# Kernel optimization log

Measured on AMD Instinct MI355X. Metric: run time of the kernel, lower is better.

## Reference

```python
import jax, jax.numpy as jnp
import numpy as np

N = 50000      # nodes
E = 800000     # edges (before self-loops)
IN = 256       # in_channels
HID = 128      # hidden_channels
OUT = 128      # out_channels
NEG_SLOPE = 0.2
EPS = 1e-16


def setup_inputs() -> dict:
    key = jax.random.key(0)
    ks = jax.random.split(key, 16)
    p = lambda k, shape: jax.random.normal(k, shape, jnp.float32) * 0.1
    return {
        "x": jax.random.normal(ks[0], (N, IN), jnp.float32),
        "edge_index": jax.random.randint(ks[1], (2, E), 0, N, dtype=jnp.int64),
        # semantic MLP
        "W1": p(ks[2], (IN, HID)), "b1": jnp.zeros((HID,), jnp.float32),
        "W2": p(ks[3], (HID, HID)), "b2": jnp.zeros((HID,), jnp.float32),
        # gat1: HID -> HID//2, heads=4, concat -> 2*HID
        "g1_W": p(ks[4], (HID, 4 * (HID // 2))),
        "g1_as": p(ks[5], (4, HID // 2)), "g1_ad": p(ks[6], (4, HID // 2)),
        "g1_b": jnp.zeros((4 * (HID // 2),), jnp.float32),
        # gat2: 2*HID -> OUT, heads=2, mean -> OUT
        "g2_W": p(ks[7], (2 * HID, 2 * OUT)),
        "g2_as": p(ks[8], (2, OUT)), "g2_ad": p(ks[9], (2, OUT)),
        "g2_b": jnp.zeros((OUT,), jnp.float32),
        # gat3: OUT -> OUT, heads=1, mean -> OUT
        "g3_W": p(ks[10], (OUT, OUT)),
        "g3_as": p(ks[11], (1, OUT)), "g3_ad": p(ks[12], (1, OUT)),
        "g3_b": jnp.zeros((OUT,), jnp.float32),
    }


def _gat(h_in, src, dst, W, a_src, a_dst, bias, heads, concat, n):
    # Linear projection into heads: [n, H, C]
    h = (h_in @ W).reshape(n, heads, -1)
    alpha_s = jnp.sum(h * a_src[None], axis=-1)  # [n, H]
    alpha_d = jnp.sum(h * a_dst[None], axis=-1)  # [n, H]
    e = jax.nn.leaky_relu(alpha_s[src] + alpha_d[dst], NEG_SLOPE)  # [E', H]
    # segment softmax over edges grouped by destination node
    m = jax.ops.segment_max(e, dst, num_segments=n)
    ex = jnp.exp(e - m[dst])
    denom = jax.ops.segment_sum(ex, dst, num_segments=n)
    alpha = ex / (denom[dst] + EPS)  # [E', H]
    msg = h[src] * alpha[..., None]  # [E', H, C]
    out = jax.ops.segment_sum(msg, dst, num_segments=n)  # [n, H, C]
    out = out.reshape(n, -1) if concat else out.mean(axis=1)
    return out + bias


def reference(x, edge_index, W1, b1, W2, b2,
              g1_W, g1_as, g1_ad, g1_b,
              g2_W, g2_as, g2_ad, g2_b,
              g3_W, g3_as, g3_ad, g3_b):
    n = x.shape[0]
    # PyG GATConv add_self_loops=True: append self-loop edges once
    loops = jnp.arange(n, dtype=edge_index.dtype)
    src = jnp.concatenate([edge_index[0], loops])
    dst = jnp.concatenate([edge_index[1], loops])
    # semantic MLP (inference: dropout = identity)
    h = jax.nn.relu(x @ W1 + b1)
    h = jax.nn.relu(h @ W2 + b2)
    h = jax.nn.elu(_gat(h, src, dst, g1_W, g1_as, g1_ad, g1_b, 4, True, n))
    h = jax.nn.elu(_gat(h, src, dst, g2_W, g2_as, g2_ad, g2_b, 2, False, n))
    h = _gat(h, src, dst, g3_W, g3_as, g3_ad, g3_b, 1, False, n)
    return h
```

## Files before the change

### kernel.cpp

```cpp
#include <hip/hip_runtime.h>
#include <math.h>


#define NEG_SLOPE 0.2f
#define EPS_DEN 1e-16f

typedef __attribute__((ext_vector_type(8))) short short8;
typedef __attribute__((ext_vector_type(4))) float f32x4;
typedef __attribute__((ext_vector_type(2))) float f32x2;
typedef __attribute__((ext_vector_type(4))) unsigned short u16x4;

__device__ inline unsigned short f2b(float f) {
  unsigned u = __builtin_bit_cast(unsigned, f);
  unsigned r = (u + 0x7fffu + ((u >> 16) & 1u)) >> 16;
  return (unsigned short)r;
}
__device__ inline float b2f(unsigned short u) {
  return __builtin_bit_cast(float, (unsigned)u << 16);
}

__device__ inline void glds16(const void* g, void* l) {
  __builtin_amdgcn_global_load_lds(
      (const __attribute__((address_space(1))) void*)g,
      (__attribute__((address_space(3))) void*)l, 16, 0, 0);
}

__device__ inline f32x2 pk_fma(f32x2 a, f32x2 b, f32x2 c) {
  f32x2 d;
  asm("v_pk_fma_f32 %0, %1, %2, %3" : "=v"(d) : "v"(a), "v"(b), "v"(c));
  return d;
}

__device__ inline void accum8(f32x2 acc2[4], const short8 r, float w) {
  const f32x2 wv = {w, w};
  const unsigned* u = (const unsigned*)&r;
#pragma unroll
  for (int p = 0; p < 4; p++) {
    const unsigned lo = u[p] << 16;
    const unsigned hi = u[p] & 0xffff0000u;
    f32x2 val = {__builtin_bit_cast(float, lo), __builtin_bit_cast(float, hi)};
    acc2[p] = pk_fma(val, wv, acc2[p]);
  }
}

template <int H>
__device__ inline void loadH(const float* p, float* v) {
  if constexpr (H == 4) {
    float4 t = *(const float4*)p;
    v[0] = t.x; v[1] = t.y; v[2] = t.z; v[3] = t.w;
  } else if constexpr (H == 2) {
    float2 t = *(const float2*)p;
    v[0] = t.x; v[1] = t.y;
  } else {
    v[0] = *p;
  }
}

template <int ACT, int OBF, int H, int CC>
__global__ __launch_bounds__(256) void mfma_gemm(
    const unsigned short* __restrict__ A, const unsigned short* __restrict__ Bt,
    const float* __restrict__ bias, float* __restrict__ Cf,
    unsigned short* __restrict__ Cb, const float* __restrict__ a_s,
    const float* __restrict__ a_d, float* __restrict__ alS,
    float* __restrict__ alD, int n, int K, int M) {
  __shared__ unsigned short As[128 * 64];
  __shared__ unsigned short Bs[128 * 64];

  const int tid = threadIdx.x;
  const int w = tid >> 6, lane = tid & 63;
  const int row0 = blockIdx.x * 128, col0 = blockIdx.y * 128;
  const int lr = lane >> 3, lg = lane & 7;
  const int lm = lane & 15, kg = lane >> 4;
  const int wm = (w >> 1) * 64, wn = (w & 1) * 64;

  f32x4 acc[4][4];
#pragma unroll
  for (int i = 0; i < 4; i++)
#pragma unroll
    for (int j = 0; j < 4; j++) acc[i][j] = {0.f, 0.f, 0.f, 0.f};

  const int swz = (lg ^ lr) << 3;

  for (int k0 = 0; k0 < K; k0 += 64) {
    __syncthreads();
#pragma unroll
    for (int it = 0; it < 4; it++) {
      const int r = w * 32 + it * 8;
      glds16(A + (size_t)(row0 + r + lr) * K + k0 + swz, &As[r * 64]);
      glds16(Bt + (size_t)(col0 + r + lr) * K + k0 + swz, &Bs[r * 64]);
    }
    __syncthreads();

#pragma unroll
    for (int kh = 0; kh < 2; kh++) {
      const int sw = ((kh * 4 + kg) ^ (lm & 7)) << 3;
      short8 aF[4], bF[4];
#pragma unroll
      for (int i = 0; i < 4; i++) {
        aF[i] = *(const short8*)&As[(wm + i * 16 + lm) * 64 + sw];
        bF[i] = *(const short8*)&Bs[(wn + i * 16 + lm) * 64 + sw];
      }
#pragma unroll
      for (int i = 0; i < 4; i++)
#pragma unroll
        for (int j = 0; j < 4; j++)
          acc[i][j] = __builtin_amdgcn_mfma_f32_16x16x32_bf16(
              aF[i], bF[j], acc[i][j], 0, 0, 0);
    }
  }

  const int r4 = kg * 4;

  if constexpr (H > 0) {
    const int head = (col0 + wn) / CC;
    const int ch0 = (col0 + wn) % CC;
    float asv[4], adv[4];
#pragma unroll
    for (int j = 0; j < 4; j++) {
      asv[j] = a_s[head * CC + ch0 + j * 16 + lm];
      adv[j] = a_d[head * CC + ch0 + j * 16 + lm];
    }
    float psA[4][4], pdA[4][4];
#pragma unroll
    for (int i = 0; i < 4; i++) {
#pragma unroll
      for (int r = 0; r < 4; r++) {
        float ps = 0.f, pd = 0.f;
#pragma unroll
        for (int j = 0; j < 4; j++) {
          ps += acc[i][j][r] * asv[j];
          pd += acc[i][j][r] * adv[j];
        }
#pragma unroll
        for (int off = 1; off < 16; off <<= 1) {
          ps += __shfl_xor(ps, off, 64);
          pd += __shfl_xor(pd, off, 64);
        }
        psA[i][r] = ps;
        pdA[i][r] = pd;
      }
    }
    if constexpr (CC == 64) {
      if (lm == 0) {
#pragma unroll
        for (int i = 0; i < 4; i++)
#pragma unroll
          for (int r = 0; r < 4; r++) {
            const int row = row0 + wm + i * 16 + r4 + r;
            if (row < n) {
              alS[(size_t)row * H + head] = psA[i][r];
              alD[(size_t)row * H + head] = pdA[i][r];
            }
          }
      }
    } else {
      __shared__ float redS[4][64];
      __shared__ float redD[4][64];
      if (lm == 0) {
#pragma unroll
        for (int i = 0; i < 4; i++)
#pragma unroll
          for (int r = 0; r < 4; r++) {
            redS[w][i * 16 + r4 + r] = psA[i][r];
            redD[w][i * 16 + r4 + r] = pdA[i][r];
          }
      }
      __syncthreads();
      if ((w & 1) == 0) {
        const int row = row0 + wm + lane;
        if (row < n) {
          const int hd = col0 / CC;
          alS[(size_t)row * H + hd] = redS[w][lane] + redS[w + 1][lane];
          alD[(size_t)row * H + hd] = redD[w][lane] + redD[w + 1][lane];
        }
      }
    }
  }

#pragma unroll
  for (int j = 0; j < 4; j++) {
    const int col = col0 + wn + j * 16 + lm;
    const float bv = bias ? bias[col] : 0.f;
#pragma unroll
    for (int i = 0; i < 4; i++) {
#pragma unroll
      for (int r = 0; r < 4; r++) {
        const int row = row0 + wm + i * 16 + r4 + r;
        if (row < n) {
          float v = acc[i][j][r] + bv;
          if (ACT == 1) v = v > 0.f ? v : 0.f;
          if (OBF)
            Cb[(size_t)row * M + col] = f2b(v);
          else
            Cf[(size_t)row * M + col] = v;
        }
      }
    }
  }
}

__global__ __launch_bounds__(256) void mlp_g1_kernel(
    const unsigned short* __restrict__ X, const unsigned short* __restrict__ W1t,
    const float* __restrict__ b1, const unsigned short* __restrict__ W2t,
    const float* __restrict__ b2, const unsigned short* __restrict__ G1Wt,
    const float* __restrict__ a_s, const float* __restrict__ a_d,
    float* __restrict__ alS, float* __restrict__ alD,
    unsigned short* __restrict__ Pb, int n) {
  __shared__ unsigned short As[128 * 64];
  __shared__ unsigned short Bs[128 * 64];
  __shared__ unsigned short H1s[128 * 136];

  const int tid = threadIdx.x;
  const int w = tid >> 6, lane = tid & 63;
  const int row0 = blockIdx.x * 128;
  const int lr = lane >> 3, lg = lane & 7;
  const int lm = lane & 15, kg = lane >> 4;
  const int wm = (w >> 1) * 64, wn = (w & 1) * 64;
  const int swz = (lg ^ lr) << 3;
  const int r4 = kg * 4;

  f32x4 acc[4][4];
#pragma unroll
  for (int i = 0; i < 4; i++)
#pragma unroll
    for (int j = 0; j < 4; j++) acc[i][j] = {0.f, 0.f, 0.f, 0.f};

  for (int k0 = 0; k0 < 256; k0 += 64) {
    __syncthreads();
#pragma unroll
    for (int it = 0; it < 4; it++) {
      const int r = w * 32 + it * 8;
      glds16(X + (size_t)(row0 + r + lr) * 256 + k0 + swz, &As[r * 64]);
      glds16(W1t + (size_t)(r + lr) * 256 + k0 + swz, &Bs[r * 64]);
    }
    __syncthreads();
#pragma unroll
    for (int kh = 0; kh < 2; kh++) {
      const int sw = ((kh * 4 + kg) ^ (lm & 7)) << 3;
      short8 aF[4], bF[4];
#pragma unroll
      for (int i = 0; i < 4; i++) {
        aF[i] = *(const short8*)&As[(wm + i * 16 + lm) * 64 + sw];
        bF[i] = *(const short8*)&Bs[(wn + i * 16 + lm) * 64 + sw];
      }
#pragma unroll
      for (int i = 0; i < 4; i++)
#pragma unroll
        for (int j = 0; j < 4; j++)
          acc[i][j] = __builtin_amdgcn_mfma_f32_16x16x32_bf16(
              aF[i], bF[j], acc[i][j], 0, 0, 0);
    }
  }

#pragma unroll
  for (int j = 0; j < 4; j++) {
    const int col = wn + j * 16 + lm;
    const float bv = b1[col];
#pragma unroll
    for (int i = 0; i < 4; i++) {
#pragma unroll
      for (int r = 0; r < 4; r++) {
        const int lrow = wm + i * 16 + r4 + r;
        float v = acc[i][j][r] + bv;
        v = v > 0.f ? v : 0.f;
        H1s[lrow * 136 + col] = f2b(v);
      }
    }
  }
#pragma unroll
  for (int i = 0; i < 4; i++)
#pragma unroll
    for (int j = 0; j < 4; j++) acc[i][j] = {0.f, 0.f, 0.f, 0.f};
  __syncthreads();

  for (int k0 = 0; k0 < 128; k0 += 64) {
    __syncthreads();
#pragma unroll
    for (int it = 0; it < 4; it++) {
      const int r = w * 32 + it * 8;
      glds16(W2t + (size_t)(r + lr) * 128 + k0 + swz, &Bs[r * 64]);
    }
    __syncthreads();
#pragma unroll
    for (int kh = 0; kh < 2; kh++) {
      const int swB = ((kh * 4 + kg) ^ (lm & 7)) << 3;
      const int kofs = k0 + (kh * 4 + kg) * 8;
      short8 aF[4], bF[4];
#pragma unroll
      for (int i = 0; i < 4; i++) {
        aF[i] = *(const short8*)&H1s[(wm + i * 16 + lm) * 136 + kofs];
        bF[i] = *(const short8*)&Bs[(wn + i * 16 + lm) * 64 + swB];
      }
#pragma unroll
      for (int i = 0; i < 4; i++)
#pragma unroll
        for (int j = 0; j < 4; j++)
          acc[i][j] = __builtin_amdgcn_mfma_f32_16x16x32_bf16(
              aF[i], bF[j], acc[i][j], 0, 0, 0);
    }
  }

  __syncthreads();
#pragma unroll
  for (int j = 0; j < 4; j++) {
    const int col = wn + j * 16 + lm;
    const float bv = b2[col];
#pragma unroll
    for (int i = 0; i < 4; i++) {
#pragma unroll
      for (int r = 0; r < 4; r++) {
        const int lrow = wm + i * 16 + r4 + r;
        float v = acc[i][j][r] + bv;
        v = v > 0.f ? v : 0.f;
        H1s[lrow * 136 + col] = f2b(v);
      }
    }
  }
  __syncthreads();

  for (int c = 0; c < 2; c++) {
#pragma unroll
    for (int i = 0; i < 4; i++)
#pragma unroll
      for (int j = 0; j < 4; j++) acc[i][j] = {0.f, 0.f, 0.f, 0.f};

    for (int k0 = 0; k0 < 128; k0 += 64) {
      __syncthreads();
#pragma unroll
      for (int it = 0; it < 4; it++) {
        const int r = w * 32 + it * 8;
        glds16(G1Wt + (size_t)(c * 128 + r + lr) * 128 + k0 + swz,
               &Bs[r * 64]);
      }
      __syncthreads();
#pragma unroll
      for (int kh = 0; kh < 2; kh++) {
        const int swB = ((kh * 4 + kg) ^ (lm & 7)) << 3;
        const int kofs = k0 + (kh * 4 + kg) * 8;
        short8 aF[4], bF[4];
#pragma unroll
        for (int i = 0; i < 4; i++) {
          aF[i] = *(const short8*)&H1s[(wm + i * 16 + lm) * 136 + kofs];
          bF[i] = *(const short8*)&Bs[(wn + i * 16 + lm) * 64 + swB];
        }
#pragma unroll
        for (int i = 0; i < 4; i++)
#pragma unroll
          for (int j = 0; j < 4; j++)
            acc[i][j] = __builtin_amdgcn_mfma_f32_16x16x32_bf16(
                aF[i], bF[j], acc[i][j], 0, 0, 0);
      }
    }

    {
      const int head = c * 2 + (wn >> 6);
      float asv[4], adv[4];
#pragma unroll
      for (int j = 0; j < 4; j++) {
        asv[j] = a_s[head * 64 + j * 16 + lm];
        adv[j] = a_d[head * 64 + j * 16 + lm];
      }
#pragma unroll
      for (int i = 0; i < 4; i++) {
#pragma unroll
        for (int r = 0; r < 4; r++) {
          float ps = 0.f, pd = 0.f;
#pragma unroll
          for (int j = 0; j < 4; j++) {
            ps += acc[i][j][r] * asv[j];
            pd += acc[i][j][r] * adv[j];
          }
#pragma unroll
          for (int off = 1; off < 16; off <<= 1) {
            ps += __shfl_xor(ps, off, 64);
            pd += __shfl_xor(pd, off, 64);
          }
          if (lm == 0) {
            const int row = row0 + wm + i * 16 + r4 + r;
            if (row < n) {
              alS[(size_t)row * 4 + head] = ps;
              alD[(size_t)row * 4 + head] = pd;
            }
          }
        }
      }
    }

#pragma unroll
    for (int j = 0; j < 4; j++) {
      const int col = c * 128 + wn + j * 16 + lm;
#pragma unroll
      for (int i = 0; i < 4; i++) {
#pragma unroll
        for (int r = 0; r < 4; r++) {
          const int row = row0 + wm + i * 16 + r4 + r;
          if (row < n) Pb[(size_t)row * 256 + col] = f2b(acc[i][j][r]);
        }
      }
    }
  }
}

struct PrepArgs {
  const float* x; unsigned short* xb; long long nx;
  const float* W[5]; unsigned short* Wt[5];
  int K[5], M[5], t0[6];
  int* deg; int* rank; const int* edst; int E; int N;
};

__global__ __launch_bounds__(256) void fused_prep_kernel(PrepArgs a) {
  const int tid = threadIdx.x, bid = blockIdx.x, nb = gridDim.x;
  const long long gt = (long long)bid * 256 + tid;
  const long long gsz = (long long)nb * 256;
  __shared__ float tt[32][33];

  const long long etot = (long long)a.E + a.N;
  for (long long i = gt; i < etot; i += gsz) {
    int d = (i < a.E) ? __builtin_nontemporal_load(a.edst + i)
                      : (int)(i - a.E);
    if ((unsigned)d < (unsigned)a.N)
      a.rank[i] = atomicAdd(&a.deg[d], 1);
  }
  for (long long i = gt * 4; i < a.nx; i += gsz * 4) {
    float4 v = *(const float4*)(a.x + i);
    u16x4 u = {f2b(v.x), f2b(v.y), f2b(v.z), f2b(v.w)};
    *(u16x4*)(a.xb + i) = u;
  }
  for (int t = bid; t < a.t0[5]; t += nb) {
    int di = 0;
    while (t >= a.t0[di + 1]) di++;
    const int local = t - a.t0[di];
    const int K = a.K[di], M = a.M[di], mtiles = M / 32;
    const int mb = (local % mtiles) * 32, kb = (local / mtiles) * 32;
    const float* W = a.W[di];
    unsigned short* Wt = a.Wt[di];
    const int tx = tid & 31, ty = tid >> 5;
    __syncthreads();
#pragma unroll
    for (int i = 0; i < 4; i++)
      tt[ty + i * 8][tx] = W[(size_t)(kb + ty + i * 8) * M + mb + tx];
    __syncthreads();
#pragma unroll
    for (int i = 0; i < 4; i++)
      Wt[(size_t)(mb + ty + i * 8) * K + kb + tx] = f2b(tt[tx][ty + i * 8]);
  }
}

__global__ __launch_bounds__(256) void block_reduce_kernel(
    const int* __restrict__ deg, int* __restrict__ bsum, int n) {
  __shared__ int s[256];
  const int t = threadIdx.x, i = blockIdx.x * 256 + t;
  s[t] = (i < n) ? deg[i] : 0;
  __syncthreads();
#pragma unroll
  for (int off = 128; off; off >>= 1) {
    if (t < off) s[t] += s[t + off];
    __syncthreads();
  }
  if (t == 0) bsum[blockIdx.x] = s[0];
}

__global__ __launch_bounds__(256) void scan_bsums_kernel(int* __restrict__ bsum,
                                                         int nb) {
  __shared__ int s[256];
  const int t = threadIdx.x;
  const int v = (t < nb) ? bsum[t] : 0;
  s[t] = v;
  __syncthreads();
#pragma unroll
  for (int off = 1; off < 256; off <<= 1) {
    int a = (t >= off) ? s[t - off] : 0;
    __syncthreads();
    s[t] += a;
    __syncthreads();
  }
  if (t < nb) bsum[t] = s[t] - v;
}

__global__ __launch_bounds__(256) void scan_final_kernel(
    const int* __restrict__ deg, const int* __restrict__ bsumx,
    int* __restrict__ rowptr, int n) {
  __shared__ int s[256];
  const int t = threadIdx.x, i = blockIdx.x * 256 + t;
  const int v = (i < n) ? deg[i] : 0;
  s[t] = v;
  __syncthreads();
#pragma unroll
  for (int off = 1; off < 256; off <<= 1) {
    int a = (t >= off) ? s[t - off] : 0;
    __syncthreads();
    s[t] += a;
    __syncthreads();
  }
  if (i < n) {
    const int base = bsumx[blockIdx.x];
    rowptr[i] = base + s[t] - v;
    if (i == n - 1) rowptr[n] = base + s[t];
  }
}

__global__ void scatter_kernel(const int* __restrict__ esrc,
                               const int* __restrict__ edst,
                               const int* __restrict__ rank,
                               const int* __restrict__ rowptr,
                               int* __restrict__ csr_src, int E, int n) {
  int i = blockIdx.x * blockDim.x + threadIdx.x;
  int tot = E + n;
  if (i >= tot) return;
  int s, d;
  if (i < E) {
    s = __builtin_nontemporal_load(esrc + i);
    d = __builtin_nontemporal_load(edst + i);
  } else {
    s = d = i - E;
  }
  if ((unsigned)d >= (unsigned)n || (unsigned)s >= (unsigned)n) return;
  int pos = rowptr[d] + __builtin_nontemporal_load(rank + i);
  csr_src[pos] = s;
}

template <int H, int C, bool CONCAT, int ACT, int OBF>
__global__ __launch_bounds__(256) void gat_fused_kernel(
    const unsigned short* __restrict__ proj, const float* __restrict__ alpha_s,
    const float* __restrict__ alpha_d, const int* __restrict__ rowptr,
    const int* __restrict__ csr_src, const float* __restrict__ bias,
    void* __restrict__ out, int n) {
  constexpr int HC = H * C;
  constexpr int ROWSPAN = HC / 8;
  constexpr int EDGES = 64 / ROWSPAN;
  constexpr int WLANES = C / 8;

  __shared__ float exs[4][64 * H];
  __shared__ int sids[4][64];

  const int wv = threadIdx.x >> 6;
  const int wid = (blockIdx.x * blockDim.x + threadIdx.x) >> 6;
  const int lane = threadIdx.x & 63;
  if (wid >= n) return;
  const int dst = wid;
  const int eslot = lane / ROWSPAN;
  const int sl = lane % ROWSPAN;
  const int h_lane = (sl * 8) / C;
  float* myex = &exs[wv][0];
  int* mysid = &sids[wv][0];

  float adv[H];
  loadH<H>(alpha_d + (size_t)dst * H, adv);
  const int rs = rowptr[dst], re = rowptr[dst + 1];

  float denomp[H];
#pragma unroll
  for (int h = 0; h < H; h++) denomp[h] = 0.f;
  f32x2 acc2[4];
#pragma unroll
  for (int p = 0; p < 4; p++) acc2[p] = {0.f, 0.f};

  const unsigned short* prow = proj + sl * 8;

  for (int base = rs; base < re; base += 64) {
    const int cnt = min(64, re - base);
    if (lane < cnt) {
      const int s = __builtin_nontemporal_load(csr_src + base + lane);
      mysid[lane] = s;
      float as[H];
      loadH<H>(alpha_s + (size_t)s * H, as);
#pragma unroll
      for (int h = 0; h < H; h++) {
        float e = as[h] + adv[h];
        e = e > 0.f ? e : NEG_SLOPE * e;
        const float ex = __expf(e);
        denomp[h] += ex;
        myex[lane * H + h] = ex;
      }
    }
    __builtin_amdgcn_wave_barrier();
    int j = eslot;
    for (; j + EDGES < cnt; j += 2 * EDGES) {
      const int s0 = mysid[j];
      const int s1 = mysid[j + EDGES];
      const float w0 = myex[j * H + h_lane];
      const float w1 = myex[(j + EDGES) * H + h_lane];
      const short8 r0 = *(const short8*)(prow + (size_t)s0 * HC);
      const short8 r1 = *(const short8*)(prow + (size_t)s1 * HC);
      accum8(acc2, r0, w0);
      accum8(acc2, r1, w1);
    }
    for (; j < cnt; j += EDGES) {
      const int s0 = mysid[j];
      const float w0 = myex[j * H + h_lane];
      const short8 r0 = *(const short8*)(prow + (size_t)s0 * HC);
      accum8(acc2, r0, w0);
    }
    __builtin_amdgcn_wave_barrier();
  }

  float acc[8];
#pragma unroll
  for (int p = 0; p < 4; p++) {
    acc[2 * p] = acc2[p].x;
    acc[2 * p + 1] = acc2[p].y;
  }

#pragma unroll
  for (int off = 32; off; off >>= 1)
#pragma unroll
    for (int h = 0; h < H; h++)
      denomp[h] += __shfl_xor(denomp[h], off, 64);
#pragma unroll
  for (int off = ROWSPAN; off < 64; off <<= 1)
#pragma unroll
    for (int k = 0; k < 8; k++) acc[k] += __shfl_xor(acc[k], off, 64);

  const float inv = 1.f / (denomp[h_lane] + EPS_DEN);
  float v[8];
#pragma unroll
  for (int k = 0; k < 8; k++) v[k] = acc[k] * inv;

  if (!CONCAT && H == 2) {
#pragma unroll
    for (int k = 0; k < 8; k++) v[k] += __shfl_xor(v[k], 16, 64);
  }

  if (CONCAT) {
    if (eslot != 0) return;
    const int c0 = sl * 8;
    float vv[8];
#pragma unroll
    for (int k = 0; k < 8; k++) {
      float t = v[k] + bias[c0 + k];
      if (ACT == 1) t = t > 0.f ? t : (__expf(t) - 1.f);
      vv[k] = t;
    }
    if (OBF) {
      short8 o;
#pragma unroll
      for (int k = 0; k < 8; k++) o[k] = (short)f2b(vv[k]);
      __builtin_nontemporal_store(
          o, (short8*)((unsigned short*)out + (size_t)dst * HC + c0));
    } else {
      float* op = (float*)out + (size_t)dst * HC + c0;
      f32x4 o0 = {vv[0], vv[1], vv[2], vv[3]};
      f32x4 o1 = {vv[4], vv[5], vv[6], vv[7]};
      __builtin_nontemporal_store(o0, (f32x4*)op);
      __builtin_nontemporal_store(o1, (f32x4*)(op + 4));
    }
  } else {
    if (eslot != 0 || sl >= WLANES) return;
    const int c0 = sl * 8;
    const float invH = 1.f / (float)H;
    float vv[8];
#pragma unroll
    for (int k = 0; k < 8; k++) {
      float t = v[k] * invH + bias[c0 + k];
      if (ACT == 1) t = t > 0.f ? t : (__expf(t) - 1.f);
      vv[k] = t;
    }
    if (OBF) {
      short8 o;
#pragma unroll
      for (int k = 0; k < 8; k++) o[k] = (short)f2b(vv[k]);
      __builtin_nontemporal_store(
          o, (short8*)((unsigned short*)out + (size_t)dst * C + c0));
    } else {
      float* op = (float*)out + (size_t)dst * C + c0;
      f32x4 o0 = {vv[0], vv[1], vv[2], vv[3]};
      f32x4 o1 = {vv[4], vv[5], vv[6], vv[7]};
      __builtin_nontemporal_store(o0, (f32x4*)op);
      __builtin_nontemporal_store(o1, (f32x4*)(op + 4));
    }
  }
}

extern "C" void kernel_launch(void* const* d_in, const int* in_sizes, int n_in,
                              void* d_out, int out_size, void* d_ws,
                              size_t ws_size, hipStream_t stream) {
  const float* x    = (const float*)d_in[0];
  const int*   ei   = (const int*)d_in[1];
  const float* W1   = (const float*)d_in[2];
  const float* b1   = (const float*)d_in[3];
  const float* W2   = (const float*)d_in[4];
  const float* b2   = (const float*)d_in[5];
  const float* g1W  = (const float*)d_in[6];
  const float* g1as = (const float*)d_in[7];
  const float* g1ad = (const float*)d_in[8];
  const float* g1b  = (const float*)d_in[9];
  const float* g2W  = (const float*)d_in[10];
  const float* g2as = (const float*)d_in[11];
  const float* g2ad = (const float*)d_in[12];
  const float* g2b  = (const float*)d_in[13];
  const float* g3W  = (const float*)d_in[14];
  const float* g3as = (const float*)d_in[15];
  const float* g3ad = (const float*)d_in[16];
  const float* g3b  = (const float*)d_in[17];

  const int N = in_sizes[0] / 256;
  const int E = in_sizes[1] / 2;
  const int Etot = E + N;
  const int NT = (N + 127) / 128;
  const int NP = NT * 128;
  const int NB = (N + 255) / 256;

  char* p = (char*)d_ws;
  unsigned short* Pb  = (unsigned short*)p; p += (size_t)NP * 256 * 2;
  unsigned short* xb  = (unsigned short*)p; p += (size_t)NP * 256 * 2;
  unsigned short* h2b = (unsigned short*)p; p += (size_t)NP * 128 * 2;
  unsigned short* W1t = (unsigned short*)p; p += (size_t)128 * 256 * 2;
  unsigned short* W2t = (unsigned short*)p; p += (size_t)128 * 128 * 2;
  unsigned short* g1Wt = (unsigned short*)p; p += (size_t)256 * 128 * 2;
  unsigned short* g2Wt = (unsigned short*)p; p += (size_t)256 * 256 * 2;
  unsigned short* g3Wt = (unsigned short*)p; p += (size_t)128 * 128 * 2;
  float* alB = (float*)p; p += (size_t)N * 14 * 4;
  float* alS1 = alB;
  float* alD1 = alB + (size_t)4 * N;
  float* alS2 = alB + (size_t)8 * N;
  float* alD2 = alB + (size_t)10 * N;
  float* alS3 = alB + (size_t)12 * N;
  float* alD3 = alB + (size_t)13 * N;
  int* deg    = (int*)p; p += (size_t)N * 4;
  int* rowptr = (int*)p; p += (size_t)(N + 1) * 4;
  int* bsum   = (int*)p; p += 256 * 4;
  int* rank   = (int*)p; p += (size_t)Etot * 4;
  int* csrsrc = (int*)p;

  const int* esrc = ei;
  const int* edst = ei + E;
  unsigned short* act1b = xb;
  unsigned short* act2b = h2b;

  hipMemsetAsync(deg, 0, (size_t)N * 4, stream);

  PrepArgs pa;
  pa.x = x; pa.xb = xb; pa.nx = (long long)N * 256;
  pa.W[0] = W1;  pa.Wt[0] = W1t;  pa.K[0] = 256; pa.M[0] = 128;
  pa.W[1] = W2;  pa.Wt[1] = W2t;  pa.K[1] = 128; pa.M[1] = 128;
  pa.W[2] = g1W; pa.Wt[2] = g1Wt; pa.K[2] = 128; pa.M[2] = 256;
  pa.W[3] = g2W; pa.Wt[3] = g2Wt; pa.K[3] = 256; pa.M[3] = 256;
  pa.W[4] = g3W; pa.Wt[4] = g3Wt; pa.K[4] = 128; pa.M[4] = 128;
  pa.t0[0] = 0;
  for (int i = 0; i < 5; i++)
    pa.t0[i + 1] = pa.t0[i] + (pa.K[i] / 32) * (pa.M[i] / 32);
  pa.deg = deg; pa.rank = rank; pa.edst = edst; pa.E = E; pa.N = N;
  fused_prep_kernel<<<512, 256, 0, stream>>>(pa);

  block_reduce_kernel<<<NB, 256, 0, stream>>>(deg, bsum, N);
  scan_bsums_kernel<<<1, 256, 0, stream>>>(bsum, NB);
  scan_final_kernel<<<NB, 256, 0, stream>>>(deg, bsum, rowptr, N);
  scatter_kernel<<<(Etot + 255) / 256, 256, 0, stream>>>(esrc, edst, rank,
                                                         rowptr, csrsrc, E, N);

  mlp_g1_kernel<<<NT, 256, 0, stream>>>(xb, W1t, b1, W2t, b2, g1Wt, g1as,
                                        g1ad, alS1, alD1, Pb, N);

  gat_fused_kernel<4, 64, true, 1, 1><<<(N + 3) / 4, 256, 0, stream>>>(
      Pb, alS1, alD1, rowptr, csrsrc, g1b, act1b, N);

  mfma_gemm<0, 1, 2, 128><<<dim3(NT, 2), 256, 0, stream>>>(
      act1b, g2Wt, nullptr, nullptr, Pb, g2as, g2ad, alS2, alD2, N, 256, 256);
  gat_fused_kernel<2, 128, false, 1, 1><<<(N + 3) / 4, 256, 0, stream>>>(
      Pb, alS2, alD2, rowptr, csrsrc, g2b, act2b, N);

  mfma_gemm<0, 1, 1, 128><<<dim3(NT, 1), 256, 0, stream>>>(
      act2b, g3Wt, nullptr, nullptr, Pb, g3as, g3ad, alS3, alD3, N, 128, 128);
  gat_fused_kernel<1, 128, false, 0, 0><<<(N + 3) / 4, 256, 0, stream>>>(
      Pb, alS3, alD3, rowptr, csrsrc, g3b, d_out, N);
}
```

Before: 449.1 us.

## Privatize degree counters per XCD to avoid cross-die atomic contention

Degree counting now uses one counter array per XCD, selected by reading the hardware XCC id, so the atomics stay within one die's L2 instead of going to shared counters across dies. The XCD id is packed into the high bits of rank. Block reduce sums the eight partial counts, scan_final turns them into per-XCD offsets, and scatter adds the matching offset. This costs an 8x larger memset and extra reads in the scan and scatter kernels, and it assumes per-node degree counts stay below 2^24.

```diff
diff --git a/kernel.cpp b/kernel.cpp
--- a/kernel.cpp
+++ b/kernel.cpp
@@ -405,7 +405,7 @@
   const float* x; unsigned short* xb; long long nx;
   const float* W[5]; unsigned short* Wt[5];
   int K[5], M[5], t0[6];
-  int* deg; int* rank; const int* edst; int E; int N;
+  int* degX; int* rank; const int* edst; int E; int N;
 };
 
 __global__ __launch_bounds__(256) void fused_prep_kernel(PrepArgs a) {
@@ -414,12 +414,17 @@
   const long long gsz = (long long)nb * 256;
   __shared__ float tt[32][33];
 
+  int xcd;
+  asm("s_getreg_b32 %0, hwreg(HW_REG_XCC_ID)" : "=s"(xcd));
+  xcd &= 7;
+  int* mydeg = a.degX + (size_t)xcd * a.N;
+
   const long long etot = (long long)a.E + a.N;
   for (long long i = gt; i < etot; i += gsz) {
     int d = (i < a.E) ? __builtin_nontemporal_load(a.edst + i)
                       : (int)(i - a.E);
     if ((unsigned)d < (unsigned)a.N)
-      a.rank[i] = atomicAdd(&a.deg[d], 1);
+      a.rank[i] = atomicAdd(&mydeg[d], 1) | (xcd << 24);
   }
   for (long long i = gt * 4; i < a.nx; i += gsz * 4) {
     float4 v = *(const float4*)(a.x + i);
@@ -447,10 +452,17 @@
 }
 
 __global__ __launch_bounds__(256) void block_reduce_kernel(
-    const int* __restrict__ deg, int* __restrict__ bsum, int n) {
+    const int* __restrict__ degX, int* __restrict__ deg,
+    int* __restrict__ bsum, int n) {
   __shared__ int s[256];
   const int t = threadIdx.x, i = blockIdx.x * 256 + t;
-  s[t] = (i < n) ? deg[i] : 0;
+  int v = 0;
+  if (i < n) {
+#pragma unroll
+    for (int x = 0; x < 8; x++) v += degX[(size_t)x * n + i];
+    deg[i] = v;
+  }
+  s[t] = v;
   __syncthreads();
 #pragma unroll
   for (int off = 128; off; off >>= 1) {
@@ -478,8 +490,8 @@
 }
 
 __global__ __launch_bounds__(256) void scan_final_kernel(
-    const int* __restrict__ deg, const int* __restrict__ bsumx,
-    int* __restrict__ rowptr, int n) {
+    const int* __restrict__ deg, int* __restrict__ degX,
+    const int* __restrict__ bsumx, int* __restrict__ rowptr, int n) {
   __shared__ int s[256];
   const int t = threadIdx.x, i = blockIdx.x * 256 + t;
   const int v = (i < n) ? deg[i] : 0;
@@ -496,6 +508,13 @@
     const int base = bsumx[blockIdx.x];
     rowptr[i] = base + s[t] - v;
     if (i == n - 1) rowptr[n] = base + s[t];
+    int run = 0;
+#pragma unroll
+    for (int x = 0; x < 8; x++) {
+      const int c = degX[(size_t)x * n + i];
+      degX[(size_t)x * n + i] = run;
+      run += c;
+    }
   }
 }
 
@@ -503,6 +522,7 @@
                                const int* __restrict__ edst,
                                const int* __restrict__ rank,
                                const int* __restrict__ rowptr,
+                               const int* __restrict__ degX,
                                int* __restrict__ csr_src, int E, int n) {
   int i = blockIdx.x * blockDim.x + threadIdx.x;
   int tot = E + n;
@@ -515,7 +535,10 @@
     s = d = i - E;
   }
   if ((unsigned)d >= (unsigned)n || (unsigned)s >= (unsigned)n) return;
-  int pos = rowptr[d] + __builtin_nontemporal_load(rank + i);
+  const int r = __builtin_nontemporal_load(rank + i);
+  const int xcd = (r >> 24) & 7;
+  const int pos =
+      rowptr[d] + degX[(size_t)xcd * n + d] + (r & 0xFFFFFF);
   csr_src[pos] = s;
 }
 
@@ -716,6 +739,7 @@
   float* alD2 = alB + (size_t)10 * N;
   float* alS3 = alB + (size_t)12 * N;
   float* alD3 = alB + (size_t)13 * N;
+  int* degX   = (int*)p; p += (size_t)8 * N * 4;
   int* deg    = (int*)p; p += (size_t)N * 4;
   int* rowptr = (int*)p; p += (size_t)(N + 1) * 4;
   int* bsum   = (int*)p; p += 256 * 4;
@@ -727,7 +751,7 @@
   unsigned short* act1b = xb;
   unsigned short* act2b = h2b;
 
-  hipMemsetAsync(deg, 0, (size_t)N * 4, stream);
+  hipMemsetAsync(degX, 0, (size_t)8 * N * 4, stream);
 
   PrepArgs pa;
   pa.x = x; pa.xb = xb; pa.nx = (long long)N * 256;
@@ -739,14 +763,14 @@
   pa.t0[0] = 0;
   for (int i = 0; i < 5; i++)
     pa.t0[i + 1] = pa.t0[i] + (pa.K[i] / 32) * (pa.M[i] / 32);
-  pa.deg = deg; pa.rank = rank; pa.edst = edst; pa.E = E; pa.N = N;
+  pa.degX = degX; pa.rank = rank; pa.edst = edst; pa.E = E; pa.N = N;
   fused_prep_kernel<<<512, 256, 0, stream>>>(pa);
 
-  block_reduce_kernel<<<NB, 256, 0, stream>>>(deg, bsum, N);
+  block_reduce_kernel<<<NB, 256, 0, stream>>>(degX, deg, bsum, N);
   scan_bsums_kernel<<<1, 256, 0, stream>>>(bsum, NB);
-  scan_final_kernel<<<NB, 256, 0, stream>>>(deg, bsum, rowptr, N);
-  scatter_kernel<<<(Etot + 255) / 256, 256, 0, stream>>>(esrc, edst, rank,
-                                                         rowptr, csrsrc, E, N);
+  scan_final_kernel<<<NB, 256, 0, stream>>>(deg, degX, bsum, rowptr, N);
+  scatter_kernel<<<(Etot + 255) / 256, 256, 0, stream>>>(
+      esrc, edst, rank, rowptr, degX, csrsrc, E, N);
 
   mlp_g1_kernel<<<NT, 256, 0, stream>>>(xb, W1t, b1, W2t, b2, g1Wt, g1as,
                                         g1ad, alS1, alD1, Pb, N);
```

New measurement: 457.4 us. Within noise of the previous version (+1.8%).

## Load MFMA operands directly from global memory instead of LDS staging

Applied to the files above, without the earlier changes.

The GEMM kernels no longer stage A and B tiles through shared memory with global_load_lds and barriers. Each lane now reads its short8 fragments straight from global memory and relies on L1/L2 caching for reuse across waves. This removes LDS traffic, barriers and LDS occupancy pressure. In exchange, global loads become redundant across the two waves sharing a tile and are no longer coalesced into whole rows, so memory latency is exposed in the MFMA loop.

```diff
diff --git a/kernel.cpp b/kernel.cpp
--- a/kernel.cpp
+++ b/kernel.cpp
@@ -17,12 +17,6 @@
 }
 __device__ inline float b2f(unsigned short u) {
   return __builtin_bit_cast(float, (unsigned)u << 16);
-}
-
-__device__ inline void glds16(const void* g, void* l) {
-  __builtin_amdgcn_global_load_lds(
-      (const __attribute__((address_space(1))) void*)g,
-      (__attribute__((address_space(3))) void*)l, 16, 0, 0);
 }
 
 __device__ inline f32x2 pk_fma(f32x2 a, f32x2 b, f32x2 c) {
@@ -63,15 +57,12 @@
     unsigned short* __restrict__ Cb, const float* __restrict__ a_s,
     const float* __restrict__ a_d, float* __restrict__ alS,
     float* __restrict__ alD, int n, int K, int M) {
-  __shared__ unsigned short As[128 * 64];
-  __shared__ unsigned short Bs[128 * 64];
-
   const int tid = threadIdx.x;
   const int w = tid >> 6, lane = tid & 63;
   const int row0 = blockIdx.x * 128, col0 = blockIdx.y * 128;
-  const int lr = lane >> 3, lg = lane & 7;
   const int lm = lane & 15, kg = lane >> 4;
   const int wm = (w >> 1) * 64, wn = (w & 1) * 64;
+  const int kofs0 = kg * 8;
 
   f32x4 acc[4][4];
 #pragma unroll
@@ -79,34 +70,28 @@
 #pragma unroll
     for (int j = 0; j < 4; j++) acc[i][j] = {0.f, 0.f, 0.f, 0.f};
 
-  const int swz = (lg ^ lr) << 3;
-
-  for (int k0 = 0; k0 < K; k0 += 64) {
-    __syncthreads();
-#pragma unroll
-    for (int it = 0; it < 4; it++) {
-      const int r = w * 32 + it * 8;
-      glds16(A + (size_t)(row0 + r + lr) * K + k0 + swz, &As[r * 64]);
-      glds16(Bt + (size_t)(col0 + r + lr) * K + k0 + swz, &Bs[r * 64]);
-    }
-    __syncthreads();
-
-#pragma unroll
-    for (int kh = 0; kh < 2; kh++) {
-      const int sw = ((kh * 4 + kg) ^ (lm & 7)) << 3;
-      short8 aF[4], bF[4];
-#pragma unroll
-      for (int i = 0; i < 4; i++) {
-        aF[i] = *(const short8*)&As[(wm + i * 16 + lm) * 64 + sw];
-        bF[i] = *(const short8*)&Bs[(wn + i * 16 + lm) * 64 + sw];
-      }
-#pragma unroll
-      for (int i = 0; i < 4; i++)
-#pragma unroll
-        for (int j = 0; j < 4; j++)
-          acc[i][j] = __builtin_amdgcn_mfma_f32_16x16x32_bf16(
-              aF[i], bF[j], acc[i][j], 0, 0, 0);
-    }
+  const unsigned short* Ap[4];
+  const unsigned short* Bp[4];
+#pragma unroll
+  for (int i = 0; i < 4; i++)
+    Ap[i] = A + (size_t)(row0 + wm + i * 16 + lm) * K + kofs0;
+#pragma unroll
+  for (int j = 0; j < 4; j++)
+    Bp[j] = Bt + (size_t)(col0 + wn + j * 16 + lm) * K + kofs0;
+
+#pragma unroll 4
+  for (int ks = 0; ks < K; ks += 32) {
+    short8 aF[4], bF[4];
+#pragma unroll
+    for (int i = 0; i < 4; i++) aF[i] = *(const short8*)(Ap[i] + ks);
+#pragma unroll
+    for (int j = 0; j < 4; j++) bF[j] = *(const short8*)(Bp[j] + ks);
+#pragma unroll
+    for (int i = 0; i < 4; i++)
+#pragma unroll
+      for (int j = 0; j < 4; j++)
+        acc[i][j] = __builtin_amdgcn_mfma_f32_16x16x32_bf16(
+            aF[i], bF[j], acc[i][j], 0, 0, 0);
   }
 
   const int r4 = kg * 4;
@@ -206,17 +191,14 @@
     const float* __restrict__ a_s, const float* __restrict__ a_d,
     float* __restrict__ alS, float* __restrict__ alD,
     unsigned short* __restrict__ Pb, int n) {
-  __shared__ unsigned short As[128 * 64];
-  __shared__ unsigned short Bs[128 * 64];
   __shared__ unsigned short H1s[128 * 136];
 
   const int tid = threadIdx.x;
   const int w = tid >> 6, lane = tid & 63;
   const int row0 = blockIdx.x * 128;
-  const int lr = lane >> 3, lg = lane & 7;
   const int lm = lane & 15, kg = lane >> 4;
   const int wm = (w >> 1) * 64, wn = (w & 1) * 64;
-  const int swz = (lg ^ lr) << 3;
+  const int kofs0 = kg * 8;
   const int r4 = kg * 4;
 
   f32x4 acc[4][4];
@@ -225,24 +207,22 @@
 #pragma unroll
     for (int j = 0; j < 4; j++) acc[i][j] = {0.f, 0.f, 0.f, 0.f};
 
-  for (int k0 = 0; k0 < 256; k0 += 64) {
-    __syncthreads();
-#pragma unroll
-    for (int it = 0; it < 4; it++) {
-      const int r = w * 32 + it * 8;
-      glds16(X + (size_t)(row0 + r + lr) * 256 + k0 + swz, &As[r * 64]);
-      glds16(W1t + (size_t)(r + lr) * 256 + k0 + swz, &Bs[r * 64]);
-    }
-    __syncthreads();
-#pragma unroll
-    for (int kh = 0; kh < 2; kh++) {
-      const int sw = ((kh * 4 + kg) ^ (lm & 7)) << 3;
+  {
+    const unsigned short* Ap[4];
+    const unsigned short* Bp[4];
+#pragma unroll
+    for (int i = 0; i < 4; i++)
+      Ap[i] = X + (size_t)(row0 + wm + i * 16 + lm) * 256 + kofs0;
+#pragma unroll
+    for (int j = 0; j < 4; j++)
+      Bp[j] = W1t + (size_t)(wn + j * 16 + lm) * 256 + kofs0;
+#pragma unroll 4
+    for (int ks = 0; ks < 256; ks += 32) {
       short8 aF[4], bF[4];
 #pragma unroll
-      for (int i = 0; i < 4; i++) {
-        aF[i] = *(const short8*)&As[(wm + i * 16 + lm) * 64 + sw];
-        bF[i] = *(const short8*)&Bs[(wn + i * 16 + lm) * 64 + sw];
-      }
+      for (int i = 0; i < 4; i++) aF[i] = *(const short8*)(Ap[i] + ks);
+#pragma unroll
+      for (int j = 0; j < 4; j++) bF[j] = *(const short8*)(Bp[j] + ks);
 #pragma unroll
       for (int i = 0; i < 4; i++)
 #pragma unroll
@@ -273,24 +253,19 @@
     for (int j = 0; j < 4; j++) acc[i][j] = {0.f, 0.f, 0.f, 0.f};
   __syncthreads();
 
-  for (int k0 = 0; k0 < 128; k0 += 64) {
-    __syncthreads();
-#pragma unroll
-    for (int it = 0; it < 4; it++) {
-      const int r = w * 32 + it * 8;
-      glds16(W2t + (size_t)(r + lr) * 128 + k0 + swz, &Bs[r * 64]);
-    }
-    __syncthreads();
-#pragma unroll
-    for (int kh = 0; kh < 2; kh++) {
-      const int swB = ((kh * 4 + kg) ^ (lm & 7)) << 3;
-      const int kofs = k0 + (kh * 4 + kg) * 8;
+  {
+    const unsigned short* Bp[4];
+#pragma unroll
+    for (int j = 0; j < 4; j++)
+      Bp[j] = W2t + (size_t)(wn + j * 16 + lm) * 128 + kofs0;
+#pragma unroll 4
+    for (int ks = 0; ks < 128; ks += 32) {
       short8 aF[4], bF[4];
 #pragma unroll
-      for (int i = 0; i < 4; i++) {
-        aF[i] = *(const short8*)&H1s[(wm + i * 16 + lm) * 136 + kofs];
-        bF[i] = *(const short8*)&Bs[(wn + i * 16 + lm) * 64 + swB];
-      }
+      for (int i = 0; i < 4; i++)
+        aF[i] = *(const short8*)&H1s[(wm + i * 16 + lm) * 136 + ks + kofs0];
+#pragma unroll
+      for (int j = 0; j < 4; j++) bF[j] = *(const short8*)(Bp[j] + ks);
 #pragma unroll
       for (int i = 0; i < 4; i++)
 #pragma unroll
@@ -299,8 +274,8 @@
               aF[i], bF[j], acc[i][j], 0, 0, 0);
     }
   }
-
   __syncthreads();
+
 #pragma unroll
   for (int j = 0; j < 4; j++) {
     const int col = wn + j * 16 + lm;
@@ -324,25 +299,19 @@
 #pragma unroll
       for (int j = 0; j < 4; j++) acc[i][j] = {0.f, 0.f, 0.f, 0.f};
 
-    for (int k0 = 0; k0 < 128; k0 += 64) {
-      __syncthreads();
-#pragma unroll
-      for (int it = 0; it < 4; it++) {
-        const int r = w * 32 + it * 8;
-        glds16(G1Wt + (size_t)(c * 128 + r + lr) * 128 + k0 + swz,
-               &Bs[r * 64]);
-      }
-      __syncthreads();
-#pragma unroll
-      for (int kh = 0; kh < 2; kh++) {
-        const int swB = ((kh * 4 + kg) ^ (lm & 7)) << 3;
-        const int kofs = k0 + (kh * 4 + kg) * 8;
+    {
+      const unsigned short* Bp[4];
+#pragma unroll
+      for (int j = 0; j < 4; j++)
+        Bp[j] = G1Wt + (size_t)(c * 128 + wn + j * 16 + lm) * 128 + kofs0;
+#pragma unroll 4
+      for (int ks = 0; ks < 128; ks += 32) {
         short8 aF[4], bF[4];
 #pragma unroll
-        for (int i = 0; i < 4; i++) {
-          aF[i] = *(const short8*)&H1s[(wm + i * 16 + lm) * 136 + kofs];
-          bF[i] = *(const short8*)&Bs[(wn + i * 16 + lm) * 64 + swB];
-        }
+        for (int i = 0; i < 4; i++)
+          aF[i] = *(const short8*)&H1s[(wm + i * 16 + lm) * 136 + ks + kofs0];
+#pragma unroll
+        for (int j = 0; j < 4; j++) bF[j] = *(const short8*)(Bp[j] + ks);
 #pragma unroll
         for (int i = 0; i < 4; i++)
 #pragma unroll
```

Result: slower. 477.7 us (+6.4%).
